# Kernel tuning notes

Hardware: AMD Instinct MI355X
Metric: run time of the kernel (lower is better)

Reference implementation:

```python
import jax, jax.numpy as jnp
import numpy as np

N = 131072   # nodes
E = 2097152  # edges (avg degree 16)
B = 4096     # subgraph (center) nodes, ntype == -1
D = 64       # feature dim (in_nfeats == all latent dims)
L = 3        # number of (local, global) RelGraphConv pairs
R = 3        # num relations
NB = 2       # num bases


def setup_inputs() -> dict:
    key = jax.random.key(0)
    ks = jax.random.split(key, 20)
    s = 0.05
    return {
        "x": jax.random.normal(ks[0], (N, D), jnp.float32),
        "src": jax.random.randint(ks[1], (E,), 0, N, jnp.int32),
        "dst": jax.random.randint(ks[2], (E,), 0, N, jnp.int32),
        "etype": jax.random.randint(ks[3], (E,), 0, R, jnp.int32),
        "mask": jax.random.uniform(ks[4], (E,), jnp.float32),
        "mask2": jax.random.uniform(ks[5], (E,), jnp.float32),
        # local RelGraphConv params (basis decomposition): W_r = sum_b C[r,b] * V[b]
        "lV": jax.random.normal(ks[6], (L, NB, D, D), jnp.float32) * s,
        "lC": jax.random.normal(ks[7], (L, R, NB), jnp.float32),
        "lW": jax.random.normal(ks[8], (L, D, D), jnp.float32) * s,   # self-loop weight
        "lB": jnp.zeros((L, D), jnp.float32),
        # global RelGraphConv params
        "gV": jax.random.normal(ks[9], (L, NB, D, D), jnp.float32) * s,
        "gC": jax.random.normal(ks[10], (L, R, NB), jnp.float32),
        "gW": jax.random.normal(ks[11], (L, D, D), jnp.float32) * s,
        "gB": jnp.zeros((L, D), jnp.float32),
        # MLP head: lin1 (sum(latent_dim)=192 -> 128), lin2 (128 -> 1)
        "w1": jax.random.normal(ks[12], (128, L * D), jnp.float32) * s,
        "b1": jnp.zeros((128,), jnp.float32),
        "w2": jax.random.normal(ks[13], (1, 128), jnp.float32) * s,
        "b2": jnp.zeros((1,), jnp.float32),
        "num_subg": B,
    }


def _rel_graph_conv(h, V, C, W, b, src, dst, etype, norm):
    """Basis-decomposed RelGraphConv with self-loop (DGL semantics, eval mode)."""
    n = h.shape[0]
    hV = jnp.einsum('nd,bdo->nbo', h, V)                  # [N, NB, D]
    coef = C[etype]                                        # [E, NB] edge-type gather
    msg = jnp.einsum('eb,ebo->eo', coef, hV[src])          # [E, D]
    msg = msg * norm[:, None]                              # per-edge norm (edge_mask)
    agg = jax.ops.segment_sum(msg, dst, num_segments=n)    # scatter-add to dst
    return agg + h @ W + b                                 # + self-loop + bias


def reference(x, src, dst, etype, mask, mask2, lV, lC, lW, lB,
              gV, gC, gW, gB, w1, b1, w2, b2, num_subg):
    # eval mode: edge_drop and Dropout(0.5) are identity
    h = x
    subg_states = []
    for i in range(L):
        h = jax.nn.elu(_rel_graph_conv(h, lV[i], lC[i], lW[i], lB[i],
                                       src, dst, etype, mask))
        # (ui_states collected in original but unused for 'center' embedding)
        h = jax.nn.leaky_relu(_rel_graph_conv(h, gV[i], gC[i], gW[i], gB[i],
                                              src, dst, etype, mask2),
                              negative_slope=0.01)
        subg_states.append(h)
    subg = jnp.concatenate(subg_states, axis=1)[:num_subg]  # subgraph-center nodes
    hid = jnp.maximum(subg @ w1.T + b1, 0.0)
    out = jax.nn.sigmoid(hid @ w2.T + b2)
    return out[:, 0]
```

## Files before the change

### kernel.cpp

```cpp
#include <hip/hip_runtime.h>
#include <math.h>

#define N_NODES 131072
#define N_EDGES 2097152
#define DIM     64
#define BSUB    4096
#define NREL    3
#define NBASES  2
#define NCB     512
#define CBSZ    8192

typedef unsigned short u16;
typedef __attribute__((ext_vector_type(8))) short bf16x8;
typedef __attribute__((ext_vector_type(4))) float f32x4;

__device__ __forceinline__ float bf2f(u16 x) {
    return __uint_as_float(((unsigned)x) << 16);
}
__device__ __forceinline__ u16 f2bf(float f) {
    unsigned u = __float_as_uint(f);
    unsigned r = (u + 0x7FFFu + ((u >> 16) & 1u)) >> 16;
    return (u16)r;
}
__device__ __forceinline__ float4 bf4_to_f4(ushort4 u) {
    return make_float4(bf2f(u.x), bf2f(u.y), bf2f(u.z), bf2f(u.w));
}
__device__ __forceinline__ ushort4 f4_to_bf4(float4 v) {
    ushort4 o; o.x = f2bf(v.x); o.y = f2bf(v.y); o.z = f2bf(v.z); o.w = f2bf(v.w);
    return o;
}


__global__ void initmark_kernel(int* __restrict__ mark, int* __restrict__ chist) {
    int i = blockIdx.x * 256 + threadIdx.x;
    if (i < N_NODES) mark[i] = (i < BSUB) ? 1 : 0;
    if (i < NCB) chist[i] = 0;
}

__global__ __launch_bounds__(256) void chist_kernel(const int* __restrict__ dst,
                                                    int* __restrict__ chist) {
    __shared__ int lh[NCB];
    int tid = threadIdx.x;
    lh[tid] = 0; lh[tid + 256] = 0;
    __syncthreads();
    int base = blockIdx.x * CBSZ;
#pragma unroll
    for (int j = 0; j < CBSZ / 1024; j++) {
        int4 d4 = *(const int4*)(dst + base + j * 1024 + tid * 4);
        atomicAdd(&lh[d4.x >> 8], 1);
        atomicAdd(&lh[d4.y >> 8], 1);
        atomicAdd(&lh[d4.z >> 8], 1);
        atomicAdd(&lh[d4.w >> 8], 1);
    }
    __syncthreads();
    atomicAdd(&chist[tid], lh[tid]);
    atomicAdd(&chist[tid + 256], lh[tid + 256]);
}

__global__ void cscan_kernel(const int* __restrict__ chist, int* __restrict__ cbase,
                             int* __restrict__ ccur, int* __restrict__ offs) {
    __shared__ int s[NCB];
    int tid = threadIdx.x;
    int v = chist[tid];
    s[tid] = v;
    __syncthreads();
    int val = v;
    for (int off = 1; off < NCB; off <<= 1) {
        int tmp = (tid >= off) ? s[tid - off] : 0;
        __syncthreads();
        val += tmp;
        s[tid] = val;
        __syncthreads();
    }
    cbase[tid] = val - v;
    ccur[tid] = val - v;
    if (tid == 0) offs[N_NODES] = N_EDGES;
}

__global__ __launch_bounds__(512) void cscatter_kernel(
    const int* __restrict__ src, const int* __restrict__ dst,
    const int* __restrict__ et, const float* __restrict__ m1,
    const float* __restrict__ m2, int* __restrict__ ccur,
    int4* __restrict__ tmp, int* __restrict__ mark) {
    __shared__ int lh[NCB];
    __shared__ int lbase[NCB];
    int tid = threadIdx.x;
    lh[tid] = 0;
    __syncthreads();
    int e0b = blockIdx.x * CBSZ;
#pragma unroll
    for (int j = 0; j < CBSZ / 2048; j++) {
        int4 d4 = *(const int4*)(dst + e0b + j * 2048 + tid * 4);
        atomicAdd(&lh[d4.x >> 8], 1);
        atomicAdd(&lh[d4.y >> 8], 1);
        atomicAdd(&lh[d4.z >> 8], 1);
        atomicAdd(&lh[d4.w >> 8], 1);
    }
    __syncthreads();
    int c = lh[tid];
    lbase[tid] = c ? atomicAdd(&ccur[tid], c) : 0;
    lh[tid] = 0;
    __syncthreads();
#pragma unroll
    for (int j = 0; j < CBSZ / 2048; j++) {
        int e0 = e0b + j * 2048 + tid * 4;
        int4  d4 = *(const int4*)(dst + e0);
        int4  s4 = *(const int4*)(src + e0);
        int4  t4 = *(const int4*)(et + e0);
        float4 a4 = *(const float4*)(m1 + e0);
        float4 b4 = *(const float4*)(m2 + e0);
#pragma unroll
        for (int k = 0; k < 4; k++) {
            int d = (&d4.x)[k];
            int s = (&s4.x)[k];
            int b = d >> 8;
            int r = atomicAdd(&lh[b], 1);
            int4 v;
            v.x = s | ((&t4.x)[k] << 20);
            v.y = __float_as_int((&a4.x)[k]);
            v.z = __float_as_int((&b4.x)[k]);
            v.w = d;
            tmp[lbase[b] + r] = v;
            if (d < BSUB) mark[s] = 1;
        }
    }
}

__global__ __launch_bounds__(256) void fscatter_kernel(
    const int4* __restrict__ tmp, const int* __restrict__ cbase,
    const int* __restrict__ chist, int* __restrict__ offs,
    int4* __restrict__ csr) {
    __shared__ int lh[256];
    __shared__ int lpre[256];
    __shared__ int s[256];
    int b = blockIdx.x;
    int tid = threadIdx.x;
    int base = cbase[b], cnt = chist[b];
    lh[tid] = 0;
    __syncthreads();
    int i = 0;
    for (; i + 1024 <= cnt; i += 1024) {
        int4 v0 = tmp[base + i + tid * 4 + 0];
        int4 v1 = tmp[base + i + tid * 4 + 1];
        int4 v2 = tmp[base + i + tid * 4 + 2];
        int4 v3 = tmp[base + i + tid * 4 + 3];
        atomicAdd(&lh[v0.w & 255], 1);
        atomicAdd(&lh[v1.w & 255], 1);
        atomicAdd(&lh[v2.w & 255], 1);
        atomicAdd(&lh[v3.w & 255], 1);
    }
    for (int k = i + tid; k < cnt; k += 256)
        atomicAdd(&lh[tmp[base + k].w & 255], 1);
    __syncthreads();
    int v = lh[tid];
    s[tid] = v;
    __syncthreads();
    int val = v;
    for (int off = 1; off < 256; off <<= 1) {
        int tq = (tid >= off) ? s[tid - off] : 0;
        __syncthreads();
        val += tq;
        s[tid] = val;
        __syncthreads();
    }
    int ex = val - v;
    lpre[tid] = ex;
    offs[b * 256 + tid] = base + ex;
    lh[tid] = 0;
    __syncthreads();
    i = 0;
    for (; i + 1024 <= cnt; i += 1024) {
        int4 v0 = tmp[base + i + tid * 4 + 0];
        int4 v1 = tmp[base + i + tid * 4 + 1];
        int4 v2 = tmp[base + i + tid * 4 + 2];
        int4 v3 = tmp[base + i + tid * 4 + 3];
        int k0 = v0.w & 255; int r0 = atomicAdd(&lh[k0], 1); csr[base + lpre[k0] + r0] = v0;
        int k1 = v1.w & 255; int r1 = atomicAdd(&lh[k1], 1); csr[base + lpre[k1] + r1] = v1;
        int k2 = v2.w & 255; int r2 = atomicAdd(&lh[k2], 1); csr[base + lpre[k2] + r2] = v2;
        int k3 = v3.w & 255; int r3 = atomicAdd(&lh[k3], 1); csr[base + lpre[k3] + r3] = v3;
    }
    for (int kk = i + tid; kk < cnt; kk += 256) {
        int4 vv = tmp[base + kk];
        int k = vv.w & 255;
        int r = atomicAdd(&lh[k], 1);
        csr[base + lpre[k] + r] = vv;
    }
}

__global__ void scan1_kernel(const int* __restrict__ cnt, int* __restrict__ scanned,
                             int* __restrict__ bsum) {
    __shared__ int s[256];
    int tid = threadIdx.x;
    int i = blockIdx.x * 256 + tid;
    int v = cnt[i];
    s[tid] = v;
    __syncthreads();
    int val = v;
    for (int off = 1; off < 256; off <<= 1) {
        int tmp = (tid >= off) ? s[tid - off] : 0;
        __syncthreads();
        val += tmp;
        s[tid] = val;
        __syncthreads();
    }
    scanned[i] = val - v;
    if (tid == 255) bsum[blockIdx.x] = val;
}

__global__ void scan2_kernel(int* __restrict__ bsum) {
    __shared__ int s[512];
    int tid = threadIdx.x;
    int v = bsum[tid];
    s[tid] = v;
    __syncthreads();
    int val = v;
    for (int off = 1; off < 512; off <<= 1) {
        int tmp = (tid >= off) ? s[tid - off] : 0;
        __syncthreads();
        val += tmp;
        s[tid] = val;
        __syncthreads();
    }
    bsum[tid] = val - v;
}

__global__ void listfill_kernel(const int* __restrict__ mark, const int* __restrict__ mpref,
                                const int* __restrict__ mbsum, int* __restrict__ list,
                                int* __restrict__ nld) {
    int i = blockIdx.x * 256 + threadIdx.x;
    int pos = mpref[i] + mbsum[blockIdx.x];
    if (mark[i]) list[pos] = i;
    if (i == N_NODES - 1) *nld = pos + mark[i];
}

__global__ void cvt_kernel(const float4* __restrict__ x, ushort4* __restrict__ hb, int n4) {
    int i = blockIdx.x * 256 + threadIdx.x;
    if (i < n4) hb[i] = f4_to_bf4(x[i]);
}

__global__ void wpack_kernel(const float* __restrict__ lV, const float* __restrict__ lW,
                             const float* __restrict__ gV, const float* __restrict__ gW,
                             u16* __restrict__ wfrag) {
    int idx = blockIdx.x * 256 + threadIdx.x;
    if (idx >= 6 * 4 * 6 * 64) return;
    int lane = idx & 63;
    int kidx = (idx >> 6) % 6;
    int nt   = (idx >> 6) / 6 % 4;
    int c    = idx / (64 * 6 * 4);
    int layer = c >> 1;
    bool isglobal = c & 1;
    const float* V = isglobal ? gV : lV;
    const float* W = isglobal ? gW : lW;
    int n = nt * 16 + (lane & 15);
    int kbase = kidx * 32 + (lane >> 4) * 8;
    u16 vals[8];
#pragma unroll
    for (int j = 0; j < 8; j++) {
        int r = kbase + j;
        float val;
        if (r < NBASES * DIM) {
            int b = r >> 6, d = r & 63;
            val = V[((layer * NBASES + b) * DIM + d) * DIM + n];
        } else {
            int d = r - NBASES * DIM;
            val = W[(layer * DIM + d) * DIM + n];
        }
        vals[j] = f2bf(val);
    }
    ushort4* o = (ushort4*)(wfrag + (size_t)idx * 8);
    o[0] = make_ushort4(vals[0], vals[1], vals[2], vals[3]);
    o[1] = make_ushort4(vals[4], vals[5], vals[6], vals[7]);
}

__global__ __launch_bounds__(256) void agg_kernel(
    const ushort4* __restrict__ hb, const int* __restrict__ offs,
    const int4* __restrict__ csr, const float* __restrict__ Cc,
    int which, ushort4* __restrict__ t, int nNodes,
    const int* __restrict__ list, const int* __restrict__ nld) {
    __shared__ int4 lmeta[4][64];
    int lane = threadIdx.x & 63;
    int wid  = threadIdx.x >> 6;
    int idx = (blockIdx.x << 2) + wid;
    int n;
    if (list) {
        if (idx >= *nld) return;
        n = list[idx];
    } else {
        if (idx >= nNodes) return;
        n = idx;
    }
    int q  = lane >> 4;
    int ql = lane & 15;
    float Ca0 = Cc[0], Cb0 = Cc[1], Ca1 = Cc[2], Cb1 = Cc[3], Ca2 = Cc[4], Cb2 = Cc[5];
    int beg = offs[n], end = offs[n + 1];
    float4 a0 = make_float4(0.f, 0.f, 0.f, 0.f);
    float4 a1 = make_float4(0.f, 0.f, 0.f, 0.f);
    for (int base = beg; base < end; base += 64) {
        int cnt = min(64, end - base);
        int pp = 0; float c0 = 0.f, c1 = 0.f;
        if (lane < cnt) {
            int4 meta = csr[base + lane];
            int et = ((unsigned)meta.x) >> 20;
            float m = __int_as_float(which ? meta.z : meta.y);
            float ca = et == 0 ? Ca0 : (et == 1 ? Ca1 : Ca2);
            float cb = et == 0 ? Cb0 : (et == 1 ? Cb1 : Cb2);
            pp = (meta.x & 0xFFFFF) << 4;
            c0 = m * ca;
            c1 = m * cb;
        }
        lmeta[wid][lane] = make_int4(pp, __float_as_int(c0), __float_as_int(c1), 0);
        for (int j = 0; j < cnt; j += 16) {
#pragma unroll
            for (int s = 0; s < 4; s++) {
                int4 md = lmeta[wid][j + (s << 2) + q];
                ushort4 rv = hb[md.x + ql];
                float4 v = bf4_to_f4(rv);
                float e0 = __int_as_float(md.y);
                float e1 = __int_as_float(md.z);
                a0.x = fmaf(e0, v.x, a0.x); a0.y = fmaf(e0, v.y, a0.y);
                a0.z = fmaf(e0, v.z, a0.z); a0.w = fmaf(e0, v.w, a0.w);
                a1.x = fmaf(e1, v.x, a1.x); a1.y = fmaf(e1, v.y, a1.y);
                a1.z = fmaf(e1, v.z, a1.z); a1.w = fmaf(e1, v.w, a1.w);
            }
        }
    }
#pragma unroll
    for (int off = 16; off < 64; off <<= 1) {
        a0.x += __shfl_xor(a0.x, off, 64); a0.y += __shfl_xor(a0.y, off, 64);
        a0.z += __shfl_xor(a0.z, off, 64); a0.w += __shfl_xor(a0.w, off, 64);
        a1.x += __shfl_xor(a1.x, off, 64); a1.y += __shfl_xor(a1.y, off, 64);
        a1.z += __shfl_xor(a1.z, off, 64); a1.w += __shfl_xor(a1.w, off, 64);
    }
    ushort4 outv = f4_to_bf4(q == 0 ? a0 : a1);
    if (q < 2)
        t[(size_t)n * 32 + (q << 4) + ql] = outv;
}

__global__ __launch_bounds__(256) void gemm_kernel(
    const u16* __restrict__ t, const u16* __restrict__ h,
    const u16* __restrict__ wfrag, const float* __restrict__ bias,
    u16* __restrict__ hout, float* __restrict__ subg, int subg_off, int act,
    const int* __restrict__ list, const int* __restrict__ nld) {
    int tid = threadIdx.x;
    int wave = tid >> 6, lane = tid & 63;
    int l16 = lane & 15, quad = lane >> 4;
    int nL = list ? *nld : 0;
    if (list && blockIdx.x * 64 >= nL) return;
    int slot0 = blockIdx.x * 64 + wave * 16;
    int myslot = slot0 + l16;
    int rowA = list ? list[min(myslot, nL - 1)] : myslot;
    const u16* trow = t + (size_t)rowA * 128;
    const u16* hrow = h + (size_t)rowA * 64;
    f32x4 acc0 = {0.f, 0.f, 0.f, 0.f};
    f32x4 acc1 = {0.f, 0.f, 0.f, 0.f};
    f32x4 acc2 = {0.f, 0.f, 0.f, 0.f};
    f32x4 acc3 = {0.f, 0.f, 0.f, 0.f};
#pragma unroll
    for (int kidx = 0; kidx < 6; kidx++) {
        bf16x8 a = (kidx < 4)
            ? *(const bf16x8*)(trow + kidx * 32 + quad * 8)
            : *(const bf16x8*)(hrow + (kidx - 4) * 32 + quad * 8);
        bf16x8 b0 = *(const bf16x8*)(wfrag + ((size_t)(0 * 6 + kidx) * 64 + lane) * 8);
        bf16x8 b1 = *(const bf16x8*)(wfrag + ((size_t)(1 * 6 + kidx) * 64 + lane) * 8);
        bf16x8 b2 = *(const bf16x8*)(wfrag + ((size_t)(2 * 6 + kidx) * 64 + lane) * 8);
        bf16x8 b3 = *(const bf16x8*)(wfrag + ((size_t)(3 * 6 + kidx) * 64 + lane) * 8);
        acc0 = __builtin_amdgcn_mfma_f32_16x16x32_bf16(a, b0, acc0, 0, 0, 0);
        acc1 = __builtin_amdgcn_mfma_f32_16x16x32_bf16(a, b1, acc1, 0, 0, 0);
        acc2 = __builtin_amdgcn_mfma_f32_16x16x32_bf16(a, b2, acc2, 0, 0, 0);
        acc3 = __builtin_amdgcn_mfma_f32_16x16x32_bf16(a, b3, acc3, 0, 0, 0);
    }
    float accs[4][4] = {
        {acc0[0], acc0[1], acc0[2], acc0[3]},
        {acc1[0], acc1[1], acc1[2], acc1[3]},
        {acc2[0], acc2[1], acc2[2], acc2[3]},
        {acc3[0], acc3[1], acc3[2], acc3[3]},
    };
#pragma unroll
    for (int nt = 0; nt < 4; nt++) {
        int col = nt * 16 + l16;
        float bcol = bias[col];
#pragma unroll
        for (int r = 0; r < 4; r++) {
            int cslot = slot0 + quad * 4 + r;
            if (list && cslot >= nL) continue;
            int row = list ? __shfl(rowA, quad * 4 + r, 64) : cslot;
            float xv = accs[nt][r] + bcol;
            float v = act ? (xv > 0.f ? xv : 0.01f * xv)
                          : (xv > 0.f ? xv : expm1f(xv));
            hout[(size_t)row * 64 + col] = f2bf(v);
            if (subg && row < BSUB)
                subg[(size_t)row * 192 + subg_off + col] = v;
        }
    }
}

__global__ __launch_bounds__(256) void head_kernel(
    const float* __restrict__ subg, const float* __restrict__ w1,
    const float* __restrict__ b1, const float* __restrict__ w2,
    const float* __restrict__ b2, float* __restrict__ out) {
    __shared__ float srow[4][192];
    int lane = threadIdx.x & 63, wid = threadIdx.x >> 6;
    int row = blockIdx.x * 4 + wid;
    const float* sr = subg + (size_t)row * 192;
    srow[wid][lane] = sr[lane];
    srow[wid][64 + lane] = sr[64 + lane];
    srow[wid][128 + lane] = sr[128 + lane];
    __syncthreads();
    float acc1 = b1[lane], acc2 = b1[64 + lane];
    const float* w1a = w1 + lane * 192;
    const float* w1b = w1 + (64 + lane) * 192;
    for (int k = 0; k < 192; k++) {
        float s = srow[wid][k];
        acc1 = fmaf(s, w1a[k], acc1);
        acc2 = fmaf(s, w1b[k], acc2);
    }
    acc1 = fmaxf(acc1, 0.f);
    acc2 = fmaxf(acc2, 0.f);
    float part = acc1 * w2[lane] + acc2 * w2[64 + lane];
    for (int off = 32; off; off >>= 1) part += __shfl_down(part, off, 64);
    if (lane == 0) out[row] = 1.f / (1.f + expf(-(part + b2[0])));
}

extern "C" void kernel_launch(void* const* d_in, const int* in_sizes, int n_in,
                              void* d_out, int out_size, void* d_ws, size_t ws_size,
                              hipStream_t stream) {
    const float* x     = (const float*)d_in[0];
    const int*   src   = (const int*)d_in[1];
    const int*   dst   = (const int*)d_in[2];
    const int*   etype = (const int*)d_in[3];
    const float* mask  = (const float*)d_in[4];
    const float* mask2 = (const float*)d_in[5];
    const float* lV = (const float*)d_in[6];
    const float* lC = (const float*)d_in[7];
    const float* lW = (const float*)d_in[8];
    const float* lB = (const float*)d_in[9];
    const float* gV = (const float*)d_in[10];
    const float* gC = (const float*)d_in[11];
    const float* gW = (const float*)d_in[12];
    const float* gB = (const float*)d_in[13];
    const float* w1 = (const float*)d_in[14];
    const float* b1 = (const float*)d_in[15];
    const float* w2 = (const float*)d_in[16];
    const float* b2 = (const float*)d_in[17];
    float* out = (float*)d_out;

    char* ws = (char*)d_ws;
    size_t off = 0;
    auto alloc = [&](size_t bytes) {
        void* p = ws + off;
        off += (bytes + 255) & ~(size_t)255;
        return p;
    };
    ushort4* h    = (ushort4*)alloc((size_t)N_NODES * 64 * 2);
    ushort4* t    = (ushort4*)alloc((size_t)N_NODES * 128 * 2);
    int4*  csr    = (int4*)alloc((size_t)N_EDGES * 16);
    int*   offs   = (int*)alloc((size_t)(N_NODES + 1) * 4);
    int*   chist  = (int*)alloc(NCB * 4);
    int*   cbase  = (int*)alloc(NCB * 4);
    int*   ccur   = (int*)alloc(NCB * 4);
    int*   bsum   = (int*)alloc(512 * 4);
    int*   mark   = (int*)alloc((size_t)N_NODES * 4);
    int*   mpref  = (int*)alloc((size_t)N_NODES * 4);
    int*   mbsum  = (int*)alloc(512 * 4);
    int*   list   = (int*)alloc((size_t)N_NODES * 4);
    int*   nld    = (int*)alloc(256);
    u16*   wfrag  = (u16*)alloc((size_t)6 * 4 * 6 * 64 * 8 * 2);
    float* subg   = (float*)alloc((size_t)BSUB * 192 * 4);
    int4*  tmp    = (int4*)t;

    initmark_kernel<<<N_NODES / 256, 256, 0, stream>>>(mark, chist);
    chist_kernel<<<N_EDGES / CBSZ, 256, 0, stream>>>(dst, chist);
    cscan_kernel<<<1, NCB, 0, stream>>>(chist, cbase, ccur, offs);
    cscatter_kernel<<<N_EDGES / CBSZ, 512, 0, stream>>>(src, dst, etype, mask, mask2,
                                                        ccur, tmp, mark);
    fscatter_kernel<<<NCB, 256, 0, stream>>>(tmp, cbase, chist, offs, csr);
    scan1_kernel<<<N_NODES / 256, 256, 0, stream>>>(mark, mpref, mbsum);
    scan2_kernel<<<1, 512, 0, stream>>>(mbsum);
    listfill_kernel<<<N_NODES / 256, 256, 0, stream>>>(mark, mpref, mbsum, list, nld);
    wpack_kernel<<<(6 * 4 * 6 * 64 + 255) / 256, 256, 0, stream>>>(lV, lW, gV, gW, wfrag);
    cvt_kernel<<<(N_NODES * 64 / 4) / 256, 256, 0, stream>>>((const float4*)x, h,
                                                             N_NODES * 64 / 4);

    const int convfrag = 4 * 6 * 64 * 8;
    for (int layer = 0; layer < 3; layer++) {
        const int* ll  = (layer == 2) ? list : nullptr;
        agg_kernel<<<N_NODES / 4, 256, 0, stream>>>(h, offs, csr,
            lC + layer * NREL * NBASES, 0, t, N_NODES, ll, nld);
        gemm_kernel<<<N_NODES / 64, 256, 0, stream>>>(
            (const u16*)t, (const u16*)h,
            wfrag + (size_t)(layer * 2 + 0) * convfrag, lB + layer * 64,
            (u16*)h, nullptr, 0, 0, ll, nld);
        int nG = (layer == 2) ? BSUB : N_NODES;
        agg_kernel<<<(nG + 3) / 4, 256, 0, stream>>>(h, offs, csr,
            gC + layer * NREL * NBASES, 1, t, nG, nullptr, nld);
        gemm_kernel<<<nG / 64, 256, 0, stream>>>(
            (const u16*)t, (const u16*)h,
            wfrag + (size_t)(layer * 2 + 1) * convfrag, gB + layer * 64,
            (u16*)h, subg, layer * 64, 1, nullptr, nld);
    }
    head_kernel<<<BSUB / 4, 256, 0, stream>>>(subg, w1, b1, w2, b2, out);
}
```

Before: 603.3 us.

## Fuse edge aggregation and MFMA transform into one kernel with ping-pong features

Merges the per-node edge aggregation and the bf16 MFMA transform into a single kernel. Each block aggregates 16 nodes into a shared-memory tile, then each wave computes one 16-column slice of the output. This removes the global round trip of the intermediate aggregate buffer and half the launches. In-place updates are no longer safe, so features now alternate between two buffers. The edge-sort scratch is aliased onto the two contiguous feature buffers. Each wave now walks four nodes sequentially, which may expose more gather latency.

After: 557.0 us. 1.08x faster.

```diff
diff --git a/kernel.cpp b/kernel.cpp
--- a/kernel.cpp
+++ b/kernel.cpp
@@ -272,125 +272,102 @@
     o[1] = make_ushort4(vals[4], vals[5], vals[6], vals[7]);
 }
 
-__global__ __launch_bounds__(256) void agg_kernel(
+__global__ __launch_bounds__(256) void aggmm_kernel(
     const ushort4* __restrict__ hb, const int* __restrict__ offs,
     const int4* __restrict__ csr, const float* __restrict__ Cc,
-    int which, ushort4* __restrict__ t, int nNodes,
-    const int* __restrict__ list, const int* __restrict__ nld) {
+    int which, const u16* __restrict__ wfrag, const float* __restrict__ bias,
+    u16* __restrict__ hout, float* __restrict__ subg, int subg_off, int act,
+    int nNodes, const int* __restrict__ list, const int* __restrict__ nld) {
     __shared__ int4 lmeta[4][64];
+    __shared__ alignas(16) ushort4 t_tile[16][34];
     int lane = threadIdx.x & 63;
     int wid  = threadIdx.x >> 6;
-    int idx = (blockIdx.x << 2) + wid;
-    int n;
-    if (list) {
-        if (idx >= *nld) return;
-        n = list[idx];
-    } else {
-        if (idx >= nNodes) return;
-        n = idx;
-    }
     int q  = lane >> 4;
     int ql = lane & 15;
+    int nld_v = list ? *nld : 0;
+    int slot0 = blockIdx.x << 4;
+    if (list && slot0 >= nld_v) return;
     float Ca0 = Cc[0], Cb0 = Cc[1], Ca1 = Cc[2], Cb1 = Cc[3], Ca2 = Cc[4], Cb2 = Cc[5];
-    int beg = offs[n], end = offs[n + 1];
-    float4 a0 = make_float4(0.f, 0.f, 0.f, 0.f);
-    float4 a1 = make_float4(0.f, 0.f, 0.f, 0.f);
-    for (int base = beg; base < end; base += 64) {
-        int cnt = min(64, end - base);
-        int pp = 0; float c0 = 0.f, c1 = 0.f;
-        if (lane < cnt) {
-            int4 meta = csr[base + lane];
-            int et = ((unsigned)meta.x) >> 20;
-            float m = __int_as_float(which ? meta.z : meta.y);
-            float ca = et == 0 ? Ca0 : (et == 1 ? Ca1 : Ca2);
-            float cb = et == 0 ? Cb0 : (et == 1 ? Cb1 : Cb2);
-            pp = (meta.x & 0xFFFFF) << 4;
-            c0 = m * ca;
-            c1 = m * cb;
+
+    for (int i = 0; i < 4; i++) {
+        int slot = slot0 + (wid << 2) + i;
+        int n = -1;
+        if (list) { if (slot < nld_v) n = list[slot]; }
+        else if (slot < nNodes) n = slot;
+        float4 a0 = make_float4(0.f, 0.f, 0.f, 0.f);
+        float4 a1 = make_float4(0.f, 0.f, 0.f, 0.f);
+        if (n >= 0) {
+            int beg = offs[n], end = offs[n + 1];
+            for (int base = beg; base < end; base += 64) {
+                int cnt = min(64, end - base);
+                int pp = 0; float c0 = 0.f, c1 = 0.f;
+                if (lane < cnt) {
+                    int4 meta = csr[base + lane];
+                    int et = ((unsigned)meta.x) >> 20;
+                    float m = __int_as_float(which ? meta.z : meta.y);
+                    float ca = et == 0 ? Ca0 : (et == 1 ? Ca1 : Ca2);
+                    float cb = et == 0 ? Cb0 : (et == 1 ? Cb1 : Cb2);
+                    pp = (meta.x & 0xFFFFF) << 4;
+                    c0 = m * ca;
+                    c1 = m * cb;
+                }
+                lmeta[wid][lane] = make_int4(pp, __float_as_int(c0), __float_as_int(c1), 0);
+                for (int j = 0; j < cnt; j += 16) {
+#pragma unroll
+                    for (int s = 0; s < 4; s++) {
+                        int4 md = lmeta[wid][j + (s << 2) + q];
+                        ushort4 rv = hb[md.x + ql];
+                        float4 v = bf4_to_f4(rv);
+                        float e0 = __int_as_float(md.y);
+                        float e1 = __int_as_float(md.z);
+                        a0.x = fmaf(e0, v.x, a0.x); a0.y = fmaf(e0, v.y, a0.y);
+                        a0.z = fmaf(e0, v.z, a0.z); a0.w = fmaf(e0, v.w, a0.w);
+                        a1.x = fmaf(e1, v.x, a1.x); a1.y = fmaf(e1, v.y, a1.y);
+                        a1.z = fmaf(e1, v.z, a1.z); a1.w = fmaf(e1, v.w, a1.w);
+                    }
+                }
+            }
+#pragma unroll
+            for (int off = 16; off < 64; off <<= 1) {
+                a0.x += __shfl_xor(a0.x, off, 64); a0.y += __shfl_xor(a0.y, off, 64);
+                a0.z += __shfl_xor(a0.z, off, 64); a0.w += __shfl_xor(a0.w, off, 64);
+                a1.x += __shfl_xor(a1.x, off, 64); a1.y += __shfl_xor(a1.y, off, 64);
+                a1.z += __shfl_xor(a1.z, off, 64); a1.w += __shfl_xor(a1.w, off, 64);
+            }
+            if (q < 2)
+                t_tile[(wid << 2) + i][(q << 4) + ql] = f4_to_bf4(q == 0 ? a0 : a1);
         }
-        lmeta[wid][lane] = make_int4(pp, __float_as_int(c0), __float_as_int(c1), 0);
-        for (int j = 0; j < cnt; j += 16) {
-#pragma unroll
-            for (int s = 0; s < 4; s++) {
-                int4 md = lmeta[wid][j + (s << 2) + q];
-                ushort4 rv = hb[md.x + ql];
-                float4 v = bf4_to_f4(rv);
-                float e0 = __int_as_float(md.y);
-                float e1 = __int_as_float(md.z);
-                a0.x = fmaf(e0, v.x, a0.x); a0.y = fmaf(e0, v.y, a0.y);
-                a0.z = fmaf(e0, v.z, a0.z); a0.w = fmaf(e0, v.w, a0.w);
-                a1.x = fmaf(e1, v.x, a1.x); a1.y = fmaf(e1, v.y, a1.y);
-                a1.z = fmaf(e1, v.z, a1.z); a1.w = fmaf(e1, v.w, a1.w);
-            }
-        }
-    }
-#pragma unroll
-    for (int off = 16; off < 64; off <<= 1) {
-        a0.x += __shfl_xor(a0.x, off, 64); a0.y += __shfl_xor(a0.y, off, 64);
-        a0.z += __shfl_xor(a0.z, off, 64); a0.w += __shfl_xor(a0.w, off, 64);
-        a1.x += __shfl_xor(a1.x, off, 64); a1.y += __shfl_xor(a1.y, off, 64);
-        a1.z += __shfl_xor(a1.z, off, 64); a1.w += __shfl_xor(a1.w, off, 64);
-    }
-    ushort4 outv = f4_to_bf4(q == 0 ? a0 : a1);
-    if (q < 2)
-        t[(size_t)n * 32 + (q << 4) + ql] = outv;
-}
-
-__global__ __launch_bounds__(256) void gemm_kernel(
-    const u16* __restrict__ t, const u16* __restrict__ h,
-    const u16* __restrict__ wfrag, const float* __restrict__ bias,
-    u16* __restrict__ hout, float* __restrict__ subg, int subg_off, int act,
-    const int* __restrict__ list, const int* __restrict__ nld) {
-    int tid = threadIdx.x;
-    int wave = tid >> 6, lane = tid & 63;
-    int l16 = lane & 15, quad = lane >> 4;
-    int nL = list ? *nld : 0;
-    if (list && blockIdx.x * 64 >= nL) return;
-    int slot0 = blockIdx.x * 64 + wave * 16;
+    }
+    __syncthreads();
+
+    int l16 = ql;
+    int quad = q;
     int myslot = slot0 + l16;
-    int rowA = list ? list[min(myslot, nL - 1)] : myslot;
-    const u16* trow = t + (size_t)rowA * 128;
-    const u16* hrow = h + (size_t)rowA * 64;
-    f32x4 acc0 = {0.f, 0.f, 0.f, 0.f};
-    f32x4 acc1 = {0.f, 0.f, 0.f, 0.f};
-    f32x4 acc2 = {0.f, 0.f, 0.f, 0.f};
-    f32x4 acc3 = {0.f, 0.f, 0.f, 0.f};
+    int rowA = list ? list[min(myslot, nld_v - 1)] : min(myslot, nNodes - 1);
+    const u16* hrow = (const u16*)hb + (size_t)rowA * 64;
+    const u16* trow = (const u16*)&t_tile[l16][0];
+    f32x4 acc = {0.f, 0.f, 0.f, 0.f};
 #pragma unroll
     for (int kidx = 0; kidx < 6; kidx++) {
         bf16x8 a = (kidx < 4)
             ? *(const bf16x8*)(trow + kidx * 32 + quad * 8)
             : *(const bf16x8*)(hrow + (kidx - 4) * 32 + quad * 8);
-        bf16x8 b0 = *(const bf16x8*)(wfrag + ((size_t)(0 * 6 + kidx) * 64 + lane) * 8);
-        bf16x8 b1 = *(const bf16x8*)(wfrag + ((size_t)(1 * 6 + kidx) * 64 + lane) * 8);
-        bf16x8 b2 = *(const bf16x8*)(wfrag + ((size_t)(2 * 6 + kidx) * 64 + lane) * 8);
-        bf16x8 b3 = *(const bf16x8*)(wfrag + ((size_t)(3 * 6 + kidx) * 64 + lane) * 8);
-        acc0 = __builtin_amdgcn_mfma_f32_16x16x32_bf16(a, b0, acc0, 0, 0, 0);
-        acc1 = __builtin_amdgcn_mfma_f32_16x16x32_bf16(a, b1, acc1, 0, 0, 0);
-        acc2 = __builtin_amdgcn_mfma_f32_16x16x32_bf16(a, b2, acc2, 0, 0, 0);
-        acc3 = __builtin_amdgcn_mfma_f32_16x16x32_bf16(a, b3, acc3, 0, 0, 0);
-    }
-    float accs[4][4] = {
-        {acc0[0], acc0[1], acc0[2], acc0[3]},
-        {acc1[0], acc1[1], acc1[2], acc1[3]},
-        {acc2[0], acc2[1], acc2[2], acc2[3]},
-        {acc3[0], acc3[1], acc3[2], acc3[3]},
-    };
-#pragma unroll
-    for (int nt = 0; nt < 4; nt++) {
-        int col = nt * 16 + l16;
-        float bcol = bias[col];
-#pragma unroll
-        for (int r = 0; r < 4; r++) {
-            int cslot = slot0 + quad * 4 + r;
-            if (list && cslot >= nL) continue;
-            int row = list ? __shfl(rowA, quad * 4 + r, 64) : cslot;
-            float xv = accs[nt][r] + bcol;
-            float v = act ? (xv > 0.f ? xv : 0.01f * xv)
-                          : (xv > 0.f ? xv : expm1f(xv));
-            hout[(size_t)row * 64 + col] = f2bf(v);
-            if (subg && row < BSUB)
-                subg[(size_t)row * 192 + subg_off + col] = v;
-        }
+        bf16x8 b = *(const bf16x8*)(wfrag + ((size_t)(wid * 6 + kidx) * 64 + lane) * 8);
+        acc = __builtin_amdgcn_mfma_f32_16x16x32_bf16(a, b, acc, 0, 0, 0);
+    }
+    int col = wid * 16 + l16;
+    float bcol = bias[col];
+#pragma unroll
+    for (int r = 0; r < 4; r++) {
+        int cslot = slot0 + quad * 4 + r;
+        if (list && cslot >= nld_v) continue;
+        int row = list ? __shfl(rowA, quad * 4 + r, 64) : cslot;
+        float xv = acc[r] + bcol;
+        float v = act ? (xv > 0.f ? xv : 0.01f * xv)
+                      : (xv > 0.f ? xv : expm1f(xv));
+        hout[(size_t)row * 64 + col] = f2bf(v);
+        if (subg && row < BSUB)
+            subg[(size_t)row * 192 + subg_off + col] = v;
     }
 }
 
@@ -451,8 +428,8 @@
         off += (bytes + 255) & ~(size_t)255;
         return p;
     };
-    ushort4* h    = (ushort4*)alloc((size_t)N_NODES * 64 * 2);
-    ushort4* t    = (ushort4*)alloc((size_t)N_NODES * 128 * 2);
+    ushort4* h0   = (ushort4*)alloc((size_t)N_NODES * 64 * 2);
+    ushort4* h1   = (ushort4*)alloc((size_t)N_NODES * 64 * 2);
     int4*  csr    = (int4*)alloc((size_t)N_EDGES * 16);
     int*   offs   = (int*)alloc((size_t)(N_NODES + 1) * 4);
     int*   chist  = (int*)alloc(NCB * 4);
@@ -466,7 +443,7 @@
     int*   nld    = (int*)alloc(256);
     u16*   wfrag  = (u16*)alloc((size_t)6 * 4 * 6 * 64 * 8 * 2);
     float* subg   = (float*)alloc((size_t)BSUB * 192 * 4);
-    int4*  tmp    = (int4*)t;
+    int4*  tmp    = (int4*)h0;
 
     initmark_kernel<<<N_NODES / 256, 256, 0, stream>>>(mark, chist);
     chist_kernel<<<N_EDGES / CBSZ, 256, 0, stream>>>(dst, chist);
@@ -478,25 +455,25 @@
     scan2_kernel<<<1, 512, 0, stream>>>(mbsum);
     listfill_kernel<<<N_NODES / 256, 256, 0, stream>>>(mark, mpref, mbsum, list, nld);
     wpack_kernel<<<(6 * 4 * 6 * 64 + 255) / 256, 256, 0, stream>>>(lV, lW, gV, gW, wfrag);
-    cvt_kernel<<<(N_NODES * 64 / 4) / 256, 256, 0, stream>>>((const float4*)x, h,
+    cvt_kernel<<<(N_NODES * 64 / 4) / 256, 256, 0, stream>>>((const float4*)x, h0,
                                                              N_NODES * 64 / 4);
 
     const int convfrag = 4 * 6 * 64 * 8;
+    ushort4* hb[2] = {h0, h1};
+    int cur = 0;
     for (int layer = 0; layer < 3; layer++) {
-        const int* ll  = (layer == 2) ? list : nullptr;
-        agg_kernel<<<N_NODES / 4, 256, 0, stream>>>(h, offs, csr,
-            lC + layer * NREL * NBASES, 0, t, N_NODES, ll, nld);
-        gemm_kernel<<<N_NODES / 64, 256, 0, stream>>>(
-            (const u16*)t, (const u16*)h,
+        const int* ll = (layer == 2) ? list : nullptr;
+        aggmm_kernel<<<N_NODES / 16, 256, 0, stream>>>(
+            hb[cur], offs, csr, lC + layer * NREL * NBASES, 0,
             wfrag + (size_t)(layer * 2 + 0) * convfrag, lB + layer * 64,
-            (u16*)h, nullptr, 0, 0, ll, nld);
+            (u16*)hb[cur ^ 1], nullptr, 0, 0, N_NODES, ll, nld);
+        cur ^= 1;
         int nG = (layer == 2) ? BSUB : N_NODES;
-        agg_kernel<<<(nG + 3) / 4, 256, 0, stream>>>(h, offs, csr,
-            gC + layer * NREL * NBASES, 1, t, nG, nullptr, nld);
-        gemm_kernel<<<nG / 64, 256, 0, stream>>>(
-            (const u16*)t, (const u16*)h,
+        aggmm_kernel<<<nG / 16, 256, 0, stream>>>(
+            hb[cur], offs, csr, gC + layer * NREL * NBASES, 1,
             wfrag + (size_t)(layer * 2 + 1) * convfrag, gB + layer * 64,
-            (u16*)h, subg, layer * 64, 1, nullptr, nld);
+            (u16*)hb[cur ^ 1], subg, layer * 64, 1, nG, nullptr, nld);
+        cur ^= 1;
     }
     head_kernel<<<BSUB / 4, 256, 0, stream>>>(subg, w1, b1, w2, b2, out);
 }
```
